# Performance work log

Measured on AMD Instinct MI355X. Metric: run time of the kernel, lower is better.

Reference implementation:

```python
import jax, jax.numpy as jnp
import numpy as np

# ---- StatDenoiser constants (init: spatial_radius=3, temporal_radius=1, alpha=0.005, spp=32) ----
SPATIAL_RADIUS = 3
TEMPORAL_RADIUS = 1
KS = 2 * SPATIAL_RADIUS + 1          # 7
KT = 2 * TEMPORAL_RADIUS + 1         # 3
N_PATCHES = KS * KS * KT             # 147
CENTER = N_PATCHES // 2              # 73 == rs*(KS*KT) + rs*KT + rt (odd sizes)
GAMMA_W = 2.907                      # scipy.stats.t.ppf(1 - 0.005/2, 32+32-2) precomputed
SIGMA_INV = jnp.asarray([0.1, 0.1, 0.1, 50.0, 50.0, 50.0, 10.0, 10.0, 10.0],
                        dtype=jnp.float32).reshape(-1, 1, 1, 1, 1)  # (9,1,1,1,1)


def shift(x):
    """Neighbors of every pixel with zero padding. x:(C,H,W,T) -> (C,P,H,W,T).
    Patch ordering (dh, dw, dt) matches torch unfold(1).unfold(2).unfold(3)."""
    C, H, W, T = x.shape
    xp = jnp.pad(x, ((0, 0), (SPATIAL_RADIUS,) * 2, (SPATIAL_RADIUS,) * 2, (TEMPORAL_RADIUS,) * 2))
    patches = [xp[:, i:i + H, j:j + W, k:k + T]
               for i in range(KS) for j in range(KS) for k in range(KT)]
    return jnp.stack(patches, axis=1)


def _compute_w(ei, ej, vi, vj):
    """Optimal weight w_ij between pixel i (center) and neighbor j."""
    d2 = (ei - ej) ** 2
    num = 2.0 * d2 + vi + vj
    den = 2.0 * (d2 + vi + vj)
    res = num / jnp.where(den == 0, 1.0, den)
    res = jnp.where((num == 0) & (den == 0), 0.5, res)
    res = jnp.where(((vi == 0) | (vj == 0)) & (ei != ej), 1.0, res)
    return res


def setup_inputs() -> dict:
    key = jax.random.key(0)
    k1, k2, k3, k4 = jax.random.split(key, 4)
    H, W, T = 64, 64, 16
    image = jax.random.uniform(k1, (3, H, W, T), dtype=jnp.float32)
    guidance = jax.random.uniform(k2, (9, H, W, T), dtype=jnp.float32)
    estimands = jax.random.uniform(k3, (3, H, W, T), dtype=jnp.float32)
    estimands_variance = jax.random.uniform(k4, (3, H, W, T), dtype=jnp.float32) * 0.01
    return {"image": image, "guidance": guidance,
            "estimands": estimands, "estimands_variance": estimands_variance}


def reference(image, guidance, estimands, estimands_variance):
    # Bilateral (range) weights from the guidance buffers.
    sg = shift(guidance)                                  # (9,P,H,W,T)
    diff2 = (sg - sg[:, CENTER:CENTER + 1]) ** 2
    bilateral = jnp.exp(-0.5 * jnp.sum(diff2 * SIGMA_INV, axis=0))   # (P,H,W,T)

    # Statistical-test membership (Welch-style t-test on estimand means/variances).
    se = shift(estimands)                                 # (3,P,H,W,T)
    sv = shift(estimands_variance)
    w_ij = _compute_w(se[:, CENTER:CENTER + 1], se,
                      sv[:, CENTER:CENTER + 1], sv)       # (3,P,H,W,T)
    arg = jnp.maximum(1.0 / (2.0 * (1.0 - w_ij)) - 1.0, 0.0)
    t_stat = jnp.where(w_ij == 1.0, jnp.inf, jnp.sqrt(arg))
    membership = jnp.all(t_stat < GAMMA_W, axis=0).astype(jnp.float32)  # (P,H,W,T)
    membership = membership.at[CENTER].set(1.0)

    # Combine: normalized (bilateral * membership) weighting of neighbor radiance.
    weights = bilateral * membership
    weights = weights / jnp.sum(weights, axis=0, keepdims=True)  # center weight==1 => sum>=1
    si = shift(image)                                      # (3,P,H,W,T)
    out = jnp.sum(si * weights[None], axis=1)              # (3,H,W,T)
    return out
```

## Files before the change

### kernel.cpp

```cpp
#include <hip/hip_runtime.h>

#define HH 64
#define WW 64
#define TT 16
#define NPIX (HH * WW * TT)
#define HALO 10
#define HWH  (HALO * HALO)
#define CH_SZ (HWH * TT)
#define NCH 15

__device__ __forceinline__ float dpp_up1(float x) {
    return __int_as_float(__builtin_amdgcn_update_dpp(
        0, __float_as_int(x), 0x111, 0xF, 0xF, true));
}
__device__ __forceinline__ float dpp_dn1(float x) {
    return __int_as_float(__builtin_amdgcn_update_dpp(
        0, __float_as_int(x), 0x101, 0xF, 0xF, true));
}

__global__ __launch_bounds__(1024, 4) void statdenoise_kernel(
    const float* __restrict__ img,
    const float* __restrict__ gui,
    const float* __restrict__ est,
    const float* __restrict__ var,
    float* __restrict__ out)
{
    __shared__ float smem[NCH * CH_SZ];

    const float SIG[9] = {0.1f, 0.1f, 0.1f, 50.0f, 50.0f, 50.0f, 10.0f, 10.0f, 10.0f};
    const float G2 = 2.907f * 2.907f;

    const int tid  = threadIdx.x;
    const int lane = tid & 63;
    const int sw   = tid >> 6;
    const int s7   = sw & 7;
    const int pg   = sw >> 3;
    const int tg   = lane & 7;
    const int hwl  = lane >> 3;
    const int t0   = tg * 2;
    const int h0   = (blockIdx.x >> 4) << 2;
    const int w0   = (blockIdx.x & 15) << 2;

#pragma unroll
    for (int rep = 0; rep < 2; ++rep) {
        const int q = tid + rep * 1024;
        if (q < CH_SZ) {
            const int t   = q & 15;
            const int hwq = q >> 4;
            const int hq  = (hwq * 205) >> 11;
            const int wq  = hwq - hq * 10;
            const int hs  = min(max(h0 - 3 + hq, 0), HH - 1);
            const int ws  = min(max(w0 - 3 + wq, 0), WW - 1);
            const int g   = (((hs << 6) + ws) << 4) + t;
#pragma unroll
            for (int c = 0; c < 9; ++c) smem[c * CH_SZ + q] = gui[c * NPIX + g];
#pragma unroll
            for (int c = 0; c < 3; ++c) {
                smem[(9 + c)  * CH_SZ + q] = est[c * NPIX + g];
                smem[(12 + c) * CH_SZ + q] = var[c * NPIX + g];
            }
        }
    }
    __syncthreads();

    const int pidx = pg * 8 + hwl;
    const int th = pidx >> 2, tw = pidx & 3;
    const int hg = h0 + th,  wg = w0 + tw;

    const int lc = (((th + 3) * 10) + (tw + 3)) * 16 + t0;
    float2 gc[9];
#pragma unroll
    for (int c = 0; c < 9; ++c) gc[c] = *(const float2*)&smem[c * CH_SZ + lc];
    float2 ec[3], vc[3];
#pragma unroll
    for (int c = 0; c < 3; ++c) {
        ec[c] = *(const float2*)&smem[(9 + c)  * CH_SZ + lc];
        vc[c] = *(const float2*)&smem[(12 + c) * CH_SZ + lc];
    }

    const bool vLo = (t0 != 0);
    const bool vHi = (t0 != 14);

    float acc[2][4] = {};

    int dh = s7 / 7 - 3, dw = s7 % 7 - 3;
    for (int r = s7; r < 49; r += 8) {
        const int lb  = ((th + dh + 3) * 10 + (tw + dw + 3)) * 16 + t0;
        const bool inb = ((unsigned)(hg + dh) < (unsigned)HH) &
                         ((unsigned)(wg + dw) < (unsigned)WW);
        const int hhc = min(max(hg + dh, 0), HH - 1);
        const int wwc = min(max(wg + dw, 0), WW - 1);
        const int gnb = (((hhc << 6) + wwc) << 4) + t0;

        float sb[2][3] = {};
#pragma unroll
        for (int c = 0; c < 9; ++c) {
            float2 m = *(const float2*)&smem[c * CH_SZ + lb];
            float nv[4] = {dpp_up1(m.y), m.x, m.y, dpp_dn1(m.x)};
#pragma unroll
            for (int e = 0; e < 2; ++e) {
                float ce = e ? gc[c].y : gc[c].x;
#pragma unroll
                for (int k = 0; k < 3; ++k) {
                    float d = ce - nv[e + k];
                    sb[e][k] = fmaf(d * d, SIG[c], sb[e][k]);
                }
            }
        }

        bool mem[2][3] = {{true, true, true}, {true, true, true}};
#pragma unroll
        for (int c = 0; c < 3; ++c) {
            float2 em = *(const float2*)&smem[(9 + c)  * CH_SZ + lb];
            float2 vm = *(const float2*)&smem[(12 + c) * CH_SZ + lb];
            float env[4] = {dpp_up1(em.y), em.x, em.y, dpp_dn1(em.x)};
            float vnv[4] = {dpp_up1(vm.y), vm.x, vm.y, dpp_dn1(vm.x)};
#pragma unroll
            for (int e = 0; e < 2; ++e) {
                float ece = e ? ec[c].y : ec[c].x;
                float vce = e ? vc[c].y : vc[c].x;
#pragma unroll
                for (int k = 0; k < 3; ++k) {
                    float d  = ece - env[e + k];
                    float d2 = d * d;
                    float V  = vce + vnv[e + k];
                    bool pass = (d2 < G2 * V) | ((d2 == 0.f) & (V == 0.f));
                    bool kill = ((vce == 0.f) | (vnv[e + k] == 0.f)) & (d2 != 0.f);
                    mem[e][k] = mem[e][k] & pass & (!kill);
                }
            }
        }

        float wt[2][3];
#pragma unroll
        for (int e = 0; e < 2; ++e) {
#pragma unroll
            for (int k = 0; k < 3; ++k) {
                bool ok = inb && mem[e][k];
                if (e == 0 && k == 0) ok = ok && vLo;
                if (e == 1 && k == 2) ok = ok && vHi;
                wt[e][k] = ok ? __expf(-0.5f * sb[e][k]) : 0.f;
            }
        }

#pragma unroll
        for (int c = 0; c < 3; ++c) {
            float2 im = *(const float2*)&img[c * NPIX + gnb];
            float iv[4] = {dpp_up1(im.y), im.x, im.y, dpp_dn1(im.x)};
#pragma unroll
            for (int e = 0; e < 2; ++e) {
                acc[e][c] = fmaf(wt[e][0], iv[e],
                            fmaf(wt[e][1], iv[e + 1],
                            fmaf(wt[e][2], iv[e + 2], acc[e][c])));
            }
        }
#pragma unroll
        for (int e = 0; e < 2; ++e)
            acc[e][3] += wt[e][0] + wt[e][1] + wt[e][2];

        dw += 8;
        while (dw > 3) { dw -= 7; ++dh; }
    }

    __syncthreads();
    float4* red = (float4*)smem;
    red[(sw * 64 + lane) * 2 + 0] = make_float4(acc[0][0], acc[0][1], acc[0][2], acc[0][3]);
    red[(sw * 64 + lane) * 2 + 1] = make_float4(acc[1][0], acc[1][1], acc[1][2], acc[1][3]);
    __syncthreads();

    if (tid < 256) {
        const int pg_ = tid >> 7, hwl_ = (tid >> 4) & 7, tg_ = (tid >> 1) & 7, e_ = tid & 1;
        float4 sum = make_float4(0.f, 0.f, 0.f, 0.f);
#pragma unroll
        for (int q = 0; q < 8; ++q) {
            const int swq = pg_ * 8 + q;
            float4 v = red[(swq * 64 + hwl_ * 8 + tg_) * 2 + e_];
            sum.x += v.x; sum.y += v.y; sum.z += v.z; sum.w += v.w;
        }
        const int pidx_ = pg_ * 8 + hwl_;
        const int th_ = pidx_ >> 2, tw_ = pidx_ & 3;
        const int px = ((((h0 + th_) << 6) + (w0 + tw_)) << 4) + tg_ * 2 + e_;
        const float inv = 1.f / sum.w;
        out[0 * NPIX + px] = sum.x * inv;
        out[1 * NPIX + px] = sum.y * inv;
        out[2 * NPIX + px] = sum.z * inv;
    }
}

extern "C" void kernel_launch(void* const* d_in, const int* in_sizes, int n_in,
                              void* d_out, int out_size, void* d_ws, size_t ws_size,
                              hipStream_t stream) {
    const float* img = (const float*)d_in[0];
    const float* gui = (const float*)d_in[1];
    const float* est = (const float*)d_in[2];
    const float* var = (const float*)d_in[3];
    float* out = (float*)d_out;

    dim3 grid(256);
    dim3 block(1024);
    statdenoise_kernel<<<grid, block, 0, stream>>>(img, gui, est, var, out);
}
```

Measured before the change: 28.74 us.

## Halve spatial tile height and spread neighbour offsets over all sixteen waves

Each block now covers a 2x4 pixel tile instead of 4x4, so the grid doubles to 512 blocks. All 16 waves of a block now share one pixel group and each wave takes a stride-16 slice of the 49 spatial offsets, instead of two pixel groups each split across 8 waves. The final reduction sums 16 partials per output instead of 8. The aim is to fill the GPU better and to shrink LDS use so that more blocks fit on a CU. The cost is a larger halo relative to the tile, which means more redundant global loads, plus uneven work per wave (4 versus 3 offsets). The raised launch-bounds occupancy hint may also limit registers.

```diff
diff --git a/kernel.cpp b/kernel.cpp
--- a/kernel.cpp
+++ b/kernel.cpp
@@ -4,9 +4,11 @@
 #define WW 64
 #define TT 16
 #define NPIX (HH * WW * TT)
-#define HALO 10
-#define HWH  (HALO * HALO)
-#define CH_SZ (HWH * TT)
+#define TH 2
+#define TW 4
+#define HALO_H (TH + 6)
+#define HALO_W (TW + 6)
+#define CH_SZ (HALO_H * HALO_W * TT)
 #define NCH 15
 
 __device__ __forceinline__ float dpp_up1(float x) {
@@ -18,7 +20,7 @@
         0, __float_as_int(x), 0x101, 0xF, 0xF, true));
 }
 
-__global__ __launch_bounds__(1024, 4) void statdenoise_kernel(
+__global__ __launch_bounds__(1024, 8) void statdenoise_kernel(
     const float* __restrict__ img,
     const float* __restrict__ gui,
     const float* __restrict__ est,
@@ -32,13 +34,11 @@
 
     const int tid  = threadIdx.x;
     const int lane = tid & 63;
-    const int sw   = tid >> 6;
-    const int s7   = sw & 7;
-    const int pg   = sw >> 3;
+    const int s    = tid >> 6;
     const int tg   = lane & 7;
     const int hwl  = lane >> 3;
     const int t0   = tg * 2;
-    const int h0   = (blockIdx.x >> 4) << 2;
+    const int h0   = (blockIdx.x >> 4) << 1;
     const int w0   = (blockIdx.x & 15) << 2;
 
 #pragma unroll
@@ -63,11 +63,11 @@
     }
     __syncthreads();
 
-    const int pidx = pg * 8 + hwl;
-    const int th = pidx >> 2, tw = pidx & 3;
+    const int th = hwl >> 2, tw = hwl & 3;
     const int hg = h0 + th,  wg = w0 + tw;
 
-    const int lc = (((th + 3) * 10) + (tw + 3)) * 16 + t0;
+    const int rowc = (th + 3) * 10 + (tw + 3);
+    const int lc = rowc * 16 + t0;
     float2 gc[9];
 #pragma unroll
     for (int c = 0; c < 9; ++c) gc[c] = *(const float2*)&smem[c * CH_SZ + lc];
@@ -83,9 +83,9 @@
 
     float acc[2][4] = {};
 
-    int dh = s7 / 7 - 3, dw = s7 % 7 - 3;
-    for (int r = s7; r < 49; r += 8) {
-        const int lb  = ((th + dh + 3) * 10 + (tw + dw + 3)) * 16 + t0;
+    int dh = s / 7 - 3, dw = s % 7 - 3;
+    for (int r = s; r < 49; r += 16) {
+        const int lb  = (rowc + dh * 10 + dw) * 16 + t0;
         const bool inb = ((unsigned)(hg + dh) < (unsigned)HH) &
                          ((unsigned)(wg + dw) < (unsigned)WW);
         const int hhc = min(max(hg + dh, 0), HH - 1);
@@ -158,28 +158,28 @@
         for (int e = 0; e < 2; ++e)
             acc[e][3] += wt[e][0] + wt[e][1] + wt[e][2];
 
-        dw += 8;
+        dw += 16;
         while (dw > 3) { dw -= 7; ++dh; }
     }
 
     __syncthreads();
     float4* red = (float4*)smem;
-    red[(sw * 64 + lane) * 2 + 0] = make_float4(acc[0][0], acc[0][1], acc[0][2], acc[0][3]);
-    red[(sw * 64 + lane) * 2 + 1] = make_float4(acc[1][0], acc[1][1], acc[1][2], acc[1][3]);
+    red[(s * 64 + lane) * 2 + 0] = make_float4(acc[0][0], acc[0][1], acc[0][2], acc[0][3]);
+    red[(s * 64 + lane) * 2 + 1] = make_float4(acc[1][0], acc[1][1], acc[1][2], acc[1][3]);
     __syncthreads();
 
-    if (tid < 256) {
-        const int pg_ = tid >> 7, hwl_ = (tid >> 4) & 7, tg_ = (tid >> 1) & 7, e_ = tid & 1;
+    if (tid < 128) {
+        const int hwl_ = tid >> 4;
+        const int tloc = tid & 15;
+        const int tg_  = tloc >> 1, e_ = tloc & 1;
         float4 sum = make_float4(0.f, 0.f, 0.f, 0.f);
 #pragma unroll
-        for (int q = 0; q < 8; ++q) {
-            const int swq = pg_ * 8 + q;
-            float4 v = red[(swq * 64 + hwl_ * 8 + tg_) * 2 + e_];
+        for (int q = 0; q < 16; ++q) {
+            float4 v = red[(q * 64 + hwl_ * 8 + tg_) * 2 + e_];
             sum.x += v.x; sum.y += v.y; sum.z += v.z; sum.w += v.w;
         }
-        const int pidx_ = pg_ * 8 + hwl_;
-        const int th_ = pidx_ >> 2, tw_ = pidx_ & 3;
-        const int px = ((((h0 + th_) << 6) + (w0 + tw_)) << 4) + tg_ * 2 + e_;
+        const int th_ = hwl_ >> 2, tw_ = hwl_ & 3;
+        const int px = ((((h0 + th_) << 6) + (w0 + tw_)) << 4) + tloc;
         const float inv = 1.f / sum.w;
         out[0 * NPIX + px] = sum.x * inv;
         out[1 * NPIX + px] = sum.y * inv;
@@ -196,7 +196,7 @@
     const float* var = (const float*)d_in[3];
     float* out = (float*)d_out;
 
-    dim3 grid(256);
+    dim3 grid(512);
     dim3 block(1024);
     statdenoise_kernel<<<grid, block, 0, stream>>>(img, gui, est, var, out);
 }
```

New measurement: 102.6 us. +257.0%, slower.
